# Performance work log

Measured on AMD Instinct MI355X. Metric: run time of the kernel, lower is better.

Reference implementation:

```python
import jax, jax.numpy as jnp
import numpy as np
from jax import lax

# SLAYER neuron / simulation constants (from netParams)
THETA = 10.0       # spike threshold
TAU_SR = 10.0      # synaptic (PSP) time constant
TAU_REF = 1.0      # refractory time constant
SCALE_REF = 2.0    # refractory scale
TAU_RHO = 1.0      # surrogate-gradient width (unused in fwd)
K_PSP = 32         # truncation length of SRM alpha kernel
K_REF = 16         # truncation length of refractory kernel

_t = np.arange(K_PSP, dtype=np.float64)
PSP_KERN = jnp.asarray((_t / TAU_SR) * np.exp(1.0 - _t / TAU_SR), jnp.float32)  # [K_PSP]
_tr = np.arange(1, K_REF + 1, dtype=np.float64)
REF_KERN = jnp.asarray(-SCALE_REF * THETA * (_tr / TAU_REF) * np.exp(1.0 - _tr / TAU_REF), jnp.float32)  # [K_REF]


def psp(x):
    """Causal temporal FIR filter with SRM alpha kernel; x: [..., T]."""
    sh = x.shape
    T = sh[-1]
    flat = x.reshape(-1, 1, T)                       # [B*, 1, T]
    k = PSP_KERN[::-1][None, None, :]                # correlation kernel (reversed)
    y = lax.conv_general_dilated(flat, k, (1,), [(K_PSP - 1, 0)])
    return y.reshape(sh)


def spike(u):
    """Threshold with refractory feedback, sequential over time. u: [..., T]."""
    uT = jnp.moveaxis(u, -1, 0)                      # [T, ...]
    buf0 = jnp.zeros(u.shape[:-1] + (K_REF,), u.dtype)

    def step(buf, ut):
        v = ut + buf[..., 0]
        s = (v >= THETA).astype(u.dtype)
        buf = jnp.concatenate([buf[..., 1:], jnp.zeros_like(buf[..., :1])], -1)
        buf = buf + s[..., None] * REF_KERN
        return buf, s

    _, sT = lax.scan(step, buf0, uT)
    return jnp.moveaxis(sT, 0, -1)


def conv_t(x, w, stride, pad):
    """2D conv applied independently per timestep. x: [N,C,H,W,T], w: [Co,C,kh,kw]."""
    N, C, H, W, T = x.shape
    xt = jnp.moveaxis(x, -1, 1).reshape(N * T, C, H, W)
    y = lax.conv_general_dilated(xt, w, (stride, stride), [(pad, pad), (pad, pad)])
    Co, Ho, Wo = y.shape[1], y.shape[2], y.shape[3]
    return jnp.moveaxis(y.reshape(N, T, Co, Ho, Wo), 1, -1)


def pool_t(x):
    """SLAYER sum-pool 2x2/s2 with weight 1.1*theta/kernel_area. x: [N,C,H,W,T]."""
    s = lax.reduce_window(x, np.float32(0.0), lax.add, (1, 1, 2, 2, 1), (1, 1, 2, 2, 1), 'VALID')
    return s * np.float32(1.1 * THETA / 4.0)


def setup_inputs() -> dict:
    key = jax.random.key(0)
    ks = jax.random.split(key, 5)
    spikeInput = (jax.random.uniform(ks[0], (4, 2, 256, 256, 50)) < 0.02).astype(jnp.float32)
    w1 = jax.random.normal(ks[1], (8, 2, 5, 5), jnp.float32) * 2.0
    w2 = jax.random.normal(ks[2], (16, 8, 3, 3), jnp.float32) * 1.5
    w3 = jax.random.normal(ks[3], (32, 16, 3, 3), jnp.float32) * 1.5
    w_fc = jax.random.normal(ks[4], (2, 32, 8, 8), jnp.float32) * 0.3
    return {"spikeInput": spikeInput, "w1": w1, "w2": w2, "w3": w3, "w_fc": w_fc}


def reference(spikeInput, w1, w2, w3, w_fc):
    x = spike(conv_t(psp(spikeInput), w1, 2, 1))   # [4,8,127,127,50]
    x = spike(pool_t(psp(x)))                      # [4,8,63,63,50]
    x = spike(conv_t(psp(x), w2, 2, 1))            # [4,16,32,32,50]
    x = spike(pool_t(psp(x)))                      # [4,16,16,16,50]
    x = spike(conv_t(psp(x), w3, 2, 1))            # [4,32,8,8,50]
    u = psp(x)
    out = jnp.einsum('ochw,nchwt->not', w_fc, u)   # dense over (C,H,W)
    return spike(out[:, :, None, None, :])         # [4,2,1,1,50]
```

## Files before the change

### kernel.cpp

```cpp
#include <hip/hip_runtime.h>
#include <cmath>

struct K32 { float k[32]; };
struct K16 { float k[16]; };

#define THETA 10.0f

__global__ __launch_bounds__(128)
void psp_kernel(const float* __restrict__ in, float* __restrict__ out,
                int nrows, K32 pk) {
  __shared__ __align__(16) float lds[64 * 50];
  const int rowBase = blockIdx.x * 64;
  const int tid = threadIdx.x;
  const int vr = min(64, nrows - rowBase);
  const int n4 = (vr * 50) >> 2;
  const float4* g4 = (const float4*)(in + (size_t)rowBase * 50);
  for (int i = tid; i < n4; i += 128) *(float4*)(&lds[4 * i]) = g4[i];
  __syncthreads();
  const int r = tid & 63;
  const int part = tid >> 6;
  const bool act = r < vr;
  float x[50];
  if (act) {
    if (part == 0) {
#pragma unroll
      for (int t = 0; t < 32; ++t) x[t] = lds[r * 50 + t];
    } else {
#pragma unroll
      for (int t = 0; t < 50; ++t) x[t] = lds[r * 50 + t];
    }
  }
  __syncthreads();
  if (act) {
    if (part == 0) {
#pragma unroll
      for (int t = 0; t < 32; ++t) {
        float a = 0.f;
#pragma unroll
        for (int k = 31; k >= 0; --k)
          if (t - k >= 0) a += x[t - k] * pk.k[k];
        lds[r * 50 + t] = a;
      }
    } else {
#pragma unroll
      for (int t = 32; t < 50; ++t) {
        float a = 0.f;
#pragma unroll
        for (int k = 31; k >= 0; --k)
          a += x[t - k] * pk.k[k];
        lds[r * 50 + t] = a;
      }
    }
  }
  __syncthreads();
  float4* o4 = (float4*)(out + (size_t)rowBase * 50);
  for (int i = tid; i < n4; i += 128) o4[i] = *(const float4*)(&lds[4 * i]);
}

template <int CIN, int COUT, int KK, int HIN, int WIN, int S1H, int S1W,
          int S2H, int S2W>
__global__ __launch_bounds__(256)
void conv_pps_kernel(const float* __restrict__ x, const float* __restrict__ w,
                     float* __restrict__ s2out, K32 pk, K16 rk) {
  constexpr int WT = 4;
  constexpr int SW = 8;
  constexpr int XR = 2 * (WT - 1) + KK;
  constexpr int GROUPS = (S1W + SW - 1) / SW;
  constexpr int NROW = COUT * 2 * SW;
  __shared__ float lds[NROW * 51];
  const int tid = threadIdx.x;
  const int wave = tid >> 6;
  const int lane = tid & 63;
  const int group = blockIdx.x % GROUPS;
  const int rest = blockIdx.x / GROUPS;
  const int hop = rest % S2H;
  const int n = rest / S2H;
  const int ho_off = wave & 1;
  const int wo_half = wave >> 1;
  const int ho = 2 * hop + ho_off;
  const int wo0 = group * SW + wo_half * WT;
  const int tt = lane < 50 ? lane : 49;

  float acc[COUT][WT] = {};
  for (int c = 0; c < CIN; ++c) {
#pragma unroll
    for (int kh = 0; kh < KK; ++kh) {
      const int hi = 2 * ho + kh - 1;
      if ((unsigned)hi >= (unsigned)HIN) continue;
      float xr[XR];
#pragma unroll
      for (int i = 0; i < XR; ++i) {
        const int wi = 2 * wo0 - 1 + i;
        xr[i] = ((unsigned)wi < (unsigned)WIN)
                    ? x[(((size_t)(n * CIN + c) * HIN + hi) * WIN + wi) * 50 + tt]
                    : 0.f;
      }
#pragma unroll
      for (int co = 0; co < COUT; ++co)
#pragma unroll
        for (int kw = 0; kw < KK; ++kw) {
          const float wv = w[((co * CIN + c) * KK + kh) * KK + kw];
#pragma unroll
          for (int wl = 0; wl < WT; ++wl)
            acc[co][wl] += xr[2 * wl + kw] * wv;
        }
    }
  }
  if (lane < 50) {
#pragma unroll
    for (int co = 0; co < COUT; ++co)
#pragma unroll
      for (int wl = 0; wl < WT; ++wl)
        lds[((co * 2 + ho_off) * SW + wo_half * WT + wl) * 51 + lane] = acc[co][wl];
  }
  __syncthreads();
  {
    const int r = tid & (NROW - 1);
    const int part = tid >> 7;
    const int wol = r & (SW - 1);
    const bool act = (group * SW + wol) < S1W;
    float xs[50];
    if (act) {
      if (part == 0) {
#pragma unroll
        for (int t = 0; t < 32; ++t) xs[t] = lds[r * 51 + t];
      } else {
#pragma unroll
        for (int t = 0; t < 50; ++t) xs[t] = lds[r * 51 + t];
      }
    }
    __syncthreads();
    if (act) {
      if (part == 0) {
        float buf[16];
#pragma unroll
        for (int j = 0; j < 16; ++j) buf[j] = 0.f;
#pragma unroll
        for (int t = 0; t < 32; ++t) {
          float v = xs[t] + buf[t & 15];
          buf[t & 15] = 0.f;
          float sp = 0.f;
          if (v >= THETA) {
            sp = 1.f;
#pragma unroll
            for (int j = 0; j < 16; ++j) buf[(t + 1 + j) & 15] += rk.k[j];
          }
          xs[t] = sp;
        }
#pragma unroll
        for (int t = 0; t < 32; ++t) {
          float a = 0.f;
#pragma unroll
          for (int k = 31; k >= 0; --k)
            if (t - k >= 0) a += xs[t - k] * pk.k[k];
          lds[r * 51 + t] = a;
        }
      } else {
        float buf[16];
#pragma unroll
        for (int j = 0; j < 16; ++j) buf[j] = 0.f;
#pragma unroll
        for (int t = 0; t < 50; ++t) {
          float v = xs[t] + buf[t & 15];
          buf[t & 15] = 0.f;
          float sp = 0.f;
          if (v >= THETA) {
            sp = 1.f;
#pragma unroll
            for (int j = 0; j < 16; ++j) buf[(t + 1 + j) & 15] += rk.k[j];
          }
          xs[t] = sp;
        }
#pragma unroll
        for (int t = 32; t < 50; ++t) {
          float a = 0.f;
#pragma unroll
          for (int k = 31; k >= 0; --k)
            a += xs[t - k] * pk.k[k];
          lds[r * 51 + t] = a;
        }
      }
    }
  }
  __syncthreads();
  if (tid < COUT * (SW / 2)) {
    const int co = tid / (SW / 2);
    const int wpl = tid % (SW / 2);
    const int wop = group * (SW / 2) + wpl;
    if (wop < S2W) {
      const int r00 = (co * 16 + 2 * wpl) * 51;
      const int r01 = (co * 16 + 2 * wpl + 1) * 51;
      const int r10 = (co * 16 + 8 + 2 * wpl) * 51;
      const int r11 = (co * 16 + 8 + 2 * wpl + 1) * 51;
      float* orow = s2out + (((size_t)(n * COUT + co) * S2H + hop) * S2W + wop) * 50;
      float buf[16];
#pragma unroll
      for (int j = 0; j < 16; ++j) buf[j] = 0.f;
      float prev = 0.f;
#pragma unroll
      for (int t = 0; t < 50; ++t) {
        const float u0 = (((lds[r00 + t] + lds[r01 + t]) + lds[r10 + t]) + lds[r11 + t]) * 2.75f;
        float v = u0 + buf[t & 15];
        buf[t & 15] = 0.f;
        float sp = 0.f;
        if (v >= THETA) {
          sp = 1.f;
#pragma unroll
          for (int j = 0; j < 16; ++j) buf[(t + 1 + j) & 15] += rk.k[j];
        }
        if (t & 1) *(float2*)(orow + t - 1) = make_float2(prev, sp);
        else prev = sp;
      }
    }
  }
}

template <int CIN, int COUT, int KK, int SW, int WT, int HIN, int WIN,
          int S1H, int S1W, int S2H, int S2W>
__global__ __launch_bounds__(256)
void conv_pps2_kernel(const float* __restrict__ x, const float* __restrict__ w,
                      float* __restrict__ s2out, K32 pk, K16 rk) {
  constexpr int XR = 2 * (WT - 1) + KK;
  constexpr int GROUPS = (S1W + SW - 1) / SW;
  constexpr int NROW = COUT * 2 * SW;
  constexpr int NROWP = COUT * (SW / 2);
  __shared__ float lds[NROW * 51];
  const int tid = threadIdx.x;
  const int wave = tid >> 6;
  const int lane = tid & 63;
  const int group = blockIdx.x % GROUPS;
  const int rest = blockIdx.x / GROUPS;
  const int hop = rest % S2H;
  const int n = rest / S2H;
  const int ho_off = wave & 1;
  const int wo_half = wave >> 1;
  const int ho = 2 * hop + ho_off;
  const int wo0 = group * SW + wo_half * WT;
  const int tt = lane < 50 ? lane : 49;

  float acc[COUT][WT] = {};
  for (int c = 0; c < CIN; ++c) {
#pragma unroll
    for (int kh = 0; kh < KK; ++kh) {
      const int hi = 2 * ho + kh - 1;
      if ((unsigned)hi >= (unsigned)HIN) continue;
      float xr[XR];
#pragma unroll
      for (int i = 0; i < XR; ++i) {
        const int wi = 2 * wo0 - 1 + i;
        xr[i] = ((unsigned)wi < (unsigned)WIN)
                    ? x[(((size_t)(n * CIN + c) * HIN + hi) * WIN + wi) * 50 + tt]
                    : 0.f;
      }
#pragma unroll
      for (int co = 0; co < COUT; ++co)
#pragma unroll
        for (int kw = 0; kw < KK; ++kw) {
          const float wv = w[((co * CIN + c) * KK + kh) * KK + kw];
#pragma unroll
          for (int wl = 0; wl < WT; ++wl)
            acc[co][wl] += xr[2 * wl + kw] * wv;
        }
    }
  }
  if (lane < 50) {
#pragma unroll
    for (int co = 0; co < COUT; ++co)
#pragma unroll
      for (int wl = 0; wl < WT; ++wl)
        lds[((co * 2 + ho_off) * SW + wo_half * WT + wl) * 51 + lane] = acc[co][wl];
  }
  __syncthreads();
  {
    const int r = tid & (NROW - 1);
    const int part = tid >> 7;
    float xs[50];
    if (part == 0) {
#pragma unroll
      for (int t = 0; t < 32; ++t) xs[t] = lds[r * 51 + t];
    } else {
#pragma unroll
      for (int t = 0; t < 50; ++t) xs[t] = lds[r * 51 + t];
    }
    __syncthreads();
    if (part == 0) {
#pragma unroll
      for (int t = 0; t < 32; ++t) {
        float a = 0.f;
#pragma unroll
        for (int k = 31; k >= 0; --k)
          if (t - k >= 0) a += xs[t - k] * pk.k[k];
        lds[r * 51 + t] = a;
      }
    } else {
#pragma unroll
      for (int t = 32; t < 50; ++t) {
        float a = 0.f;
#pragma unroll
        for (int k = 31; k >= 0; --k)
          a += xs[t - k] * pk.k[k];
        lds[r * 51 + t] = a;
      }
    }
  }
  __syncthreads();
  if (tid < NROW) {
    float buf[16];
#pragma unroll
    for (int j = 0; j < 16; ++j) buf[j] = 0.f;
#pragma unroll
    for (int t = 0; t < 50; ++t) {
      float v = lds[tid * 51 + t] + buf[t & 15];
      buf[t & 15] = 0.f;
      float sp = 0.f;
      if (v >= THETA) {
        sp = 1.f;
#pragma unroll
        for (int j = 0; j < 16; ++j) buf[(t + 1 + j) & 15] += rk.k[j];
      }
      lds[tid * 51 + t] = sp;
    }
  }
  __syncthreads();
  {
    const int r = tid & (NROWP - 1);
    const int part = tid >> 5;
    const bool act = part < 2;
    const int co = r / (SW / 2);
    const int wpl = r % (SW / 2);
    const int r00 = ((co * 2) * SW + 2 * wpl) * 51;
    const int r01 = r00 + 51;
    const int r10 = ((co * 2 + 1) * SW + 2 * wpl) * 51;
    const int r11 = r10 + 51;
    float xs[50];
    if (act) {
      if (part == 0) {
#pragma unroll
        for (int t = 0; t < 32; ++t)
          xs[t] = (((lds[r00 + t] + lds[r01 + t]) + lds[r10 + t]) + lds[r11 + t]) * 2.75f;
      } else {
#pragma unroll
        for (int t = 0; t < 50; ++t)
          xs[t] = (((lds[r00 + t] + lds[r01 + t]) + lds[r10 + t]) + lds[r11 + t]) * 2.75f;
      }
    }
    __syncthreads();
    if (act) {
      if (part == 0) {
#pragma unroll
        for (int t = 0; t < 32; ++t) {
          float a = 0.f;
#pragma unroll
          for (int k = 31; k >= 0; --k)
            if (t - k >= 0) a += xs[t - k] * pk.k[k];
          lds[r00 + t] = a;
        }
      } else {
#pragma unroll
        for (int t = 32; t < 50; ++t) {
          float a = 0.f;
#pragma unroll
          for (int k = 31; k >= 0; --k)
            a += xs[t - k] * pk.k[k];
          lds[r00 + t] = a;
        }
      }
    }
  }
  __syncthreads();
  if (tid < NROWP) {
    const int co = tid / (SW / 2);
    const int wpl = tid % (SW / 2);
    const int wop = group * (SW / 2) + wpl;
    if (wop < S2W) {
      const int r00 = ((co * 2) * SW + 2 * wpl) * 51;
      float* orow = s2out + (((size_t)(n * COUT + co) * S2H + hop) * S2W + wop) * 50;
      float buf[16];
#pragma unroll
      for (int j = 0; j < 16; ++j) buf[j] = 0.f;
      float prev = 0.f;
#pragma unroll
      for (int t = 0; t < 50; ++t) {
        float v = lds[r00 + t] + buf[t & 15];
        buf[t & 15] = 0.f;
        float sp = 0.f;
        if (v >= THETA) {
          sp = 1.f;
#pragma unroll
          for (int j = 0; j < 16; ++j) buf[(t + 1 + j) & 15] += rk.k[j];
        }
        if (t & 1) *(float2*)(orow + t - 1) = make_float2(prev, sp);
        else prev = sp;
      }
    }
  }
}

template <int CIN, int COUT, int KK, int WT, int HIN, int WIN, int HOUT, int WOUT>
__global__ __launch_bounds__(256)
void conv_fir_spike_kernel(const float* __restrict__ x, const float* __restrict__ w,
                           float* __restrict__ s, K32 pk, K16 rk) {
  constexpr int XR = 2 * (WT - 1) + KK;
  constexpr int TW = 4 * WT;
  constexpr int GROUPS = (WOUT + TW - 1) / TW;
  constexpr int NROW = COUT * TW;
  __shared__ float lds[NROW * 51];
  const int tid = threadIdx.x;
  const int wave = tid >> 6;
  const int lane = tid & 63;
  const int group = blockIdx.x % GROUPS;
  const int rest = blockIdx.x / GROUPS;
  const int ho = rest % HOUT;
  const int n = rest / HOUT;
  const int wo0 = group * TW + wave * WT;
  const int tt = lane < 50 ? lane : 49;

  float acc[COUT][WT] = {};
  for (int c = 0; c < CIN; ++c) {
#pragma unroll
    for (int kh = 0; kh < KK; ++kh) {
      const int hi = 2 * ho + kh - 1;
      if ((unsigned)hi >= (unsigned)HIN) continue;
      float xr[XR];
#pragma unroll
      for (int i = 0; i < XR; ++i) {
        const int wi = 2 * wo0 - 1 + i;
        xr[i] = ((unsigned)wi < (unsigned)WIN)
                    ? x[(((size_t)(n * CIN + c) * HIN + hi) * WIN + wi) * 50 + tt]
                    : 0.f;
      }
#pragma unroll
      for (int co = 0; co < COUT; ++co)
#pragma unroll
        for (int kw = 0; kw < KK; ++kw) {
          const float wv = w[((co * CIN + c) * KK + kh) * KK + kw];
#pragma unroll
          for (int wl = 0; wl < WT; ++wl)
            acc[co][wl] += xr[2 * wl + kw] * wv;
        }
    }
  }

  if (lane < 50) {
#pragma unroll
    for (int co = 0; co < COUT; ++co)
#pragma unroll
      for (int wl = 0; wl < WT; ++wl)
        lds[(co * TW + wave * WT + wl) * 51 + lane] = acc[co][wl];
  }
  __syncthreads();
  {
    const int r = tid % NROW;
    const int part = tid / NROW;
    const int wol = r % TW;
    const bool act = (part < 2) && (group * TW + wol < WOUT);
    float xs[50];
    if (act) {
      if (part == 0) {
#pragma unroll
        for (int t = 0; t < 25; ++t) xs[t] = lds[r * 51 + t];
      } else {
#pragma unroll
        for (int t = 0; t < 50; ++t) xs[t] = lds[r * 51 + t];
      }
    }
    __syncthreads();
    if (act) {
      if (part == 0) {
#pragma unroll
        for (int t = 0; t < 25; ++t) {
          float a = 0.f;
#pragma unroll
          for (int k = 31; k >= 0; --k)
            if (t - k >= 0) a += xs[t - k] * pk.k[k];
          lds[r * 51 + t] = a;
        }
      } else {
#pragma unroll
        for (int t = 25; t < 50; ++t) {
          float a = 0.f;
#pragma unroll
          for (int k = 31; k >= 0; --k)
            if (t - k >= 0) a += xs[t - k] * pk.k[k];
          lds[r * 51 + t] = a;
        }
      }
    }
  }
  __syncthreads();
  if (tid < NROW) {
    const int co = tid / TW;
    const int wol = tid - co * TW;
    const int wo = group * TW + wol;
    if (wo < WOUT) {
      float* orow = s + (((size_t)(n * COUT + co) * HOUT + ho) * WOUT + wo) * 50;
      float buf[16];
#pragma unroll
      for (int j = 0; j < 16; ++j) buf[j] = 0.f;
      float prev = 0.f;
#pragma unroll
      for (int t = 0; t < 50; ++t) {
        float v = lds[tid * 51 + t] + buf[t & 15];
        buf[t & 15] = 0.f;
        float sp = 0.f;
        if (v >= THETA) {
          sp = 1.f;
#pragma unroll
          for (int j = 0; j < 16; ++j) buf[(t + 1 + j) & 15] += rk.k[j];
        }
        if (t & 1) *(float2*)(orow + t - 1) = make_float2(prev, sp);
        else prev = sp;
      }
    }
  }
}

__global__ __launch_bounds__(512)
void fc_fir_spike_kernel(const float* __restrict__ w, const float* __restrict__ s,
                         float* __restrict__ out, K32 pk, K16 rk) {
  __shared__ float lds[8 * 51];
  const int tid = threadIdx.x;
  const int wave = tid >> 6, lane = tid & 63;
  const int o = wave & 1, n = wave >> 1;
  const int tt = lane < 50 ? lane : 49;
  const float* wrow = w + (size_t)o * 2048;
  const float* ub = s + (size_t)n * 2048 * 50;
  float acc = 0.f;
#pragma unroll 32
  for (int i = 0; i < 2048; ++i) acc += wrow[i] * ub[(size_t)i * 50 + tt];
  if (lane < 50) lds[wave * 51 + lane] = acc;
  __syncthreads();
  {
    const int r = tid & 7;
    const int part = tid >> 3;
    const bool act = part < 2;
    float xs[50];
    if (act) {
      if (part == 0) {
#pragma unroll
        for (int t = 0; t < 25; ++t) xs[t] = lds[r * 51 + t];
      } else {
#pragma unroll
        for (int t = 0; t < 50; ++t) xs[t] = lds[r * 51 + t];
      }
    }
    __syncthreads();
    if (act) {
      if (part == 0) {
#pragma unroll
        for (int t = 0; t < 25; ++t) {
          float a = 0.f;
#pragma unroll
          for (int k = 31; k >= 0; --k)
            if (t - k >= 0) a += xs[t - k] * pk.k[k];
          lds[r * 51 + t] = a;
        }
      } else {
#pragma unroll
        for (int t = 25; t < 50; ++t) {
          float a = 0.f;
#pragma unroll
          for (int k = 31; k >= 0; --k)
            if (t - k >= 0) a += xs[t - k] * pk.k[k];
          lds[r * 51 + t] = a;
        }
      }
    }
  }
  __syncthreads();
  if (tid < 8) {
    float buf[16];
#pragma unroll
    for (int j = 0; j < 16; ++j) buf[j] = 0.f;
#pragma unroll
    for (int t = 0; t < 50; ++t) {
      float v = lds[tid * 51 + t] + buf[t & 15];
      buf[t & 15] = 0.f;
      float sp = 0.f;
      if (v >= THETA) {
        sp = 1.f;
#pragma unroll
        for (int j = 0; j < 16; ++j) buf[(t + 1 + j) & 15] += rk.k[j];
      }
      out[tid * 50 + t] = sp;
    }
  }
}

extern "C" void kernel_launch(void* const* d_in, const int* in_sizes, int n_in,
                              void* d_out, int out_size, void* d_ws, size_t ws_size,
                              hipStream_t stream) {
  const float* xin = (const float*)d_in[0];
  const float* w1  = (const float*)d_in[1];
  const float* w2  = (const float*)d_in[2];
  const float* w3  = (const float*)d_in[3];
  const float* wfc = (const float*)d_in[4];
  float* out = (float*)d_out;

  float* R0 = (float*)d_ws;
  float* R1 = R0 + 26214400;

  K32 pk;
  for (int k = 0; k < 32; ++k)
    pk.k[k] = (float)(((double)k / 10.0) * exp(1.0 - (double)k / 10.0));
  K16 rk;
  for (int j = 0; j < 16; ++j) {
    const double tr = (double)(j + 1);
    rk.k[j] = (float)(-2.0 * 10.0 * tr * exp(1.0 - tr));
  }

  psp_kernel<<<8192, 128, 0, stream>>>(xin, R0, 524288, pk);
  conv_pps_kernel<2, 8, 5, 256, 256, 127, 127, 63, 63>
      <<<4 * 63 * 16, 256, 0, stream>>>(R0, w1, R1, pk, rk);
  conv_pps2_kernel<8, 16, 3, 4, 2, 63, 63, 32, 32, 16, 16>
      <<<4 * 16 * 8, 256, 0, stream>>>(R1, w2, R0, pk, rk);
  conv_fir_spike_kernel<16, 32, 3, 1, 16, 16, 8, 8>
      <<<4 * 8 * 2, 256, 0, stream>>>(R0, w3, R1, pk, rk);
  fc_fir_spike_kernel<<<1, 512, 0, stream>>>(wfc, R1, out, pk, rk);
}
```

Before: 479.3 us.

## Commute input PSP filter past conv1 and fuse it into conv kernel

Removes the standalone PSP pass over the raw input and instead applies the temporal FIR to conv1 outputs inside the fused conv/spike kernel, relying on linearity so psp and conv commute. This eliminates a full read/write round trip of the large input tensor and filters fewer elements. The two thread halves' time ranges are rebalanced with a split point to even per-thread FIR work, at the cost of more registers per thread.

```diff
diff --git a/kernel.cpp b/kernel.cpp
--- a/kernel.cpp
+++ b/kernel.cpp
@@ -5,57 +5,6 @@
 struct K16 { float k[16]; };
 
 #define THETA 10.0f
-
-__global__ __launch_bounds__(128)
-void psp_kernel(const float* __restrict__ in, float* __restrict__ out,
-                int nrows, K32 pk) {
-  __shared__ __align__(16) float lds[64 * 50];
-  const int rowBase = blockIdx.x * 64;
-  const int tid = threadIdx.x;
-  const int vr = min(64, nrows - rowBase);
-  const int n4 = (vr * 50) >> 2;
-  const float4* g4 = (const float4*)(in + (size_t)rowBase * 50);
-  for (int i = tid; i < n4; i += 128) *(float4*)(&lds[4 * i]) = g4[i];
-  __syncthreads();
-  const int r = tid & 63;
-  const int part = tid >> 6;
-  const bool act = r < vr;
-  float x[50];
-  if (act) {
-    if (part == 0) {
-#pragma unroll
-      for (int t = 0; t < 32; ++t) x[t] = lds[r * 50 + t];
-    } else {
-#pragma unroll
-      for (int t = 0; t < 50; ++t) x[t] = lds[r * 50 + t];
-    }
-  }
-  __syncthreads();
-  if (act) {
-    if (part == 0) {
-#pragma unroll
-      for (int t = 0; t < 32; ++t) {
-        float a = 0.f;
-#pragma unroll
-        for (int k = 31; k >= 0; --k)
-          if (t - k >= 0) a += x[t - k] * pk.k[k];
-        lds[r * 50 + t] = a;
-      }
-    } else {
-#pragma unroll
-      for (int t = 32; t < 50; ++t) {
-        float a = 0.f;
-#pragma unroll
-        for (int k = 31; k >= 0; --k)
-          a += x[t - k] * pk.k[k];
-        lds[r * 50 + t] = a;
-      }
-    }
-  }
-  __syncthreads();
-  float4* o4 = (float4*)(out + (size_t)rowBase * 50);
-  for (int i = tid; i < n4; i += 128) o4[i] = *(const float4*)(&lds[4 * i]);
-}
 
 template <int CIN, int COUT, int KK, int HIN, int WIN, int S1H, int S1W,
           int S2H, int S2W>
@@ -67,6 +16,7 @@
   constexpr int XR = 2 * (WT - 1) + KK;
   constexpr int GROUPS = (S1W + SW - 1) / SW;
   constexpr int NROW = COUT * 2 * SW;
+  constexpr int T0 = 39;
   __shared__ float lds[NROW * 51];
   const int tid = threadIdx.x;
   const int wave = tid >> 6;
@@ -123,7 +73,7 @@
     if (act) {
       if (part == 0) {
 #pragma unroll
-        for (int t = 0; t < 32; ++t) xs[t] = lds[r * 51 + t];
+        for (int t = 0; t < T0; ++t) xs[t] = lds[r * 51 + t];
       } else {
 #pragma unroll
         for (int t = 0; t < 50; ++t) xs[t] = lds[r * 51 + t];
@@ -132,12 +82,29 @@
     __syncthreads();
     if (act) {
       if (part == 0) {
+        float us[T0];
+#pragma unroll
+        for (int t = 0; t < 32; ++t) {
+          float a = 0.f;
+#pragma unroll
+          for (int k = 31; k >= 0; --k)
+            if (t - k >= 0) a += xs[t - k] * pk.k[k];
+          us[t] = a;
+        }
+#pragma unroll
+        for (int t = 32; t < T0; ++t) {
+          float a = 0.f;
+#pragma unroll
+          for (int k = 31; k >= 0; --k)
+            a += xs[t - k] * pk.k[k];
+          us[t] = a;
+        }
         float buf[16];
 #pragma unroll
         for (int j = 0; j < 16; ++j) buf[j] = 0.f;
 #pragma unroll
-        for (int t = 0; t < 32; ++t) {
-          float v = xs[t] + buf[t & 15];
+        for (int t = 0; t < T0; ++t) {
+          float v = us[t] + buf[t & 15];
           buf[t & 15] = 0.f;
           float sp = 0.f;
           if (v >= THETA) {
@@ -145,23 +112,48 @@
 #pragma unroll
             for (int j = 0; j < 16; ++j) buf[(t + 1 + j) & 15] += rk.k[j];
           }
-          xs[t] = sp;
+          us[t] = sp;
         }
 #pragma unroll
         for (int t = 0; t < 32; ++t) {
           float a = 0.f;
 #pragma unroll
           for (int k = 31; k >= 0; --k)
+            if (t - k >= 0) a += us[t - k] * pk.k[k];
+          lds[r * 51 + t] = a;
+        }
+#pragma unroll
+        for (int t = 32; t < T0; ++t) {
+          float a = 0.f;
+#pragma unroll
+          for (int k = 31; k >= 0; --k)
+            a += us[t - k] * pk.k[k];
+          lds[r * 51 + t] = a;
+        }
+      } else {
+        float us[50];
+#pragma unroll
+        for (int t = 0; t < 32; ++t) {
+          float a = 0.f;
+#pragma unroll
+          for (int k = 31; k >= 0; --k)
             if (t - k >= 0) a += xs[t - k] * pk.k[k];
-          lds[r * 51 + t] = a;
-        }
-      } else {
+          us[t] = a;
+        }
+#pragma unroll
+        for (int t = 32; t < 50; ++t) {
+          float a = 0.f;
+#pragma unroll
+          for (int k = 31; k >= 0; --k)
+            a += xs[t - k] * pk.k[k];
+          us[t] = a;
+        }
         float buf[16];
 #pragma unroll
         for (int j = 0; j < 16; ++j) buf[j] = 0.f;
 #pragma unroll
         for (int t = 0; t < 50; ++t) {
-          float v = xs[t] + buf[t & 15];
+          float v = us[t] + buf[t & 15];
           buf[t & 15] = 0.f;
           float sp = 0.f;
           if (v >= THETA) {
@@ -169,14 +161,14 @@
 #pragma unroll
             for (int j = 0; j < 16; ++j) buf[(t + 1 + j) & 15] += rk.k[j];
           }
-          xs[t] = sp;
-        }
-#pragma unroll
-        for (int t = 32; t < 50; ++t) {
-          float a = 0.f;
-#pragma unroll
-          for (int k = 31; k >= 0; --k)
-            a += xs[t - k] * pk.k[k];
+          us[t] = sp;
+        }
+#pragma unroll
+        for (int t = T0; t < 50; ++t) {
+          float a = 0.f;
+#pragma unroll
+          for (int k = 31; k >= 0; --k)
+            a += us[t - k] * pk.k[k];
           lds[r * 51 + t] = a;
         }
       }
@@ -609,9 +601,8 @@
     rk.k[j] = (float)(-2.0 * 10.0 * tr * exp(1.0 - tr));
   }
 
-  psp_kernel<<<8192, 128, 0, stream>>>(xin, R0, 524288, pk);
   conv_pps_kernel<2, 8, 5, 256, 256, 127, 127, 63, 63>
-      <<<4 * 63 * 16, 256, 0, stream>>>(R0, w1, R1, pk, rk);
+      <<<4 * 63 * 16, 256, 0, stream>>>(xin, w1, R1, pk, rk);
   conv_pps2_kernel<8, 16, 3, 4, 2, 63, 63, 32, 32, 16, 16>
       <<<4 * 16 * 8, 256, 0, stream>>>(R1, w2, R0, pk, rk);
   conv_fir_spike_kernel<16, 32, 3, 1, 16, 16, 8, 8>
```

Measured after the change: 464.8 us. -3.0%, faster.
